# Kernel optimization log

Measured on AMD Instinct MI355X. Metric: run time of the kernel, lower is better.

Reference implementation:

```python
import jax, jax.numpy as jnp
import numpy as np

H = 1024      # hidden_size
I = 512       # moe_intermediate_size
E = 8         # n_routed_experts
K = 2         # num_experts_per_tok
SI = I * 2    # shared expert intermediate (n_shared_experts=2)
B, S = 2, 1024


def setup_inputs() -> dict:
    key = jax.random.key(0)
    ks = jax.random.split(key, 9)
    s = 0.02
    return {
        "x": jax.random.normal(ks[0], (B, S, H), jnp.float32),
        "gate_w": jax.random.normal(ks[1], (E, H), jnp.float32) * s,
        "lb_bias": jnp.zeros((E,), jnp.float32),
        "expert_gate_w": jax.random.normal(ks[2], (E, I, H), jnp.float32) * s,
        "expert_up_w": jax.random.normal(ks[3], (E, I, H), jnp.float32) * s,
        "expert_down_w": jax.random.normal(ks[4], (E, H, I), jnp.float32) * s,
        "shared_gate_w": jax.random.normal(ks[5], (SI, H), jnp.float32) * s,
        "shared_up_w": jax.random.normal(ks[6], (SI, H), jnp.float32) * s,
        "shared_down_w": jax.random.normal(ks[7], (H, SI), jnp.float32) * s,
    }


def _mlp(x, gw, uw, dw):
    # SwiGLU: down( silu(gate(x)) * up(x) )
    return (jax.nn.silu(x @ gw.T) * (x @ uw.T)) @ dw.T


def reference(x, gate_w, lb_bias, expert_gate_w, expert_up_w, expert_down_w,
              shared_gate_w, shared_up_w, shared_down_w):
    b, s, h = x.shape
    xf = x.reshape(-1, h)                                   # [T, H]
    # --- SimpleRouter (sigmoid scoring) ---
    logits = xf @ gate_w.T + lb_bias                        # [T, E]
    scores = jax.nn.sigmoid(logits.astype(jnp.float32))
    topw, topi = jax.lax.top_k(scores, K)                   # [T, K]
    topw = (topw / (topw.sum(-1, keepdims=True) + 1e-8)).astype(x.dtype)
    # --- _process_local: per-expert dispatch/compute/combine ---
    # Faithful to torch source: expert_weights[mask].mean(dim=-1) collapses to a
    # SCALAR per expert (mean routing weight over all tokens sent to that expert).
    out = jnp.zeros_like(xf)
    for e in range(E):
        m = (topi == e)                                     # [T, K]
        sel = m.any(axis=-1)                                # [T]
        cnt = m.sum()
        wmean = (topw * m).sum() / jnp.maximum(cnt, 1).astype(topw.dtype)
        y = _mlp(xf, expert_gate_w[e], expert_up_w[e], expert_down_w[e])  # [T, H]
        out = out + jnp.where(sel[:, None], y * wmean, jnp.zeros((), x.dtype))
    out = out.reshape(b, s, h)
    # --- shared experts ---
    out = out + _mlp(x, shared_gate_w, shared_up_w, shared_down_w)
    return out
```

## Files before the change

kernel.cpp:

```cpp
#include <hip/hip_runtime.h>

#define H_DIM 1024
#define I_DIM 512
#define NE 8
#define SI_DIM 1024
#define NT 2048
#define NS 4096

typedef __bf16 bf16;
typedef __bf16 bf16x4 __attribute__((ext_vector_type(4)));
typedef __bf16 bf16x8 __attribute__((ext_vector_type(8)));
typedef float f32x4 __attribute__((ext_vector_type(4)));

#define W_GU 0
#define W_DN 8388608ull
#define W_SGU 12582912ull
#define W_SDN 14680064ull
#define W_TOT 15728640ull

#define NWB 15360
#define NXB 2048
#define NRB 512

#define OFF_CNT 0
#define OFF_WM 64
#define OFF_BASE 128
#define OFF_TOPI 1024
#define OFF_TOPW (OFF_TOPI + NT * 8)
#define OFF_GSLOT (OFF_TOPW + NT * 8)
#define OFF_LISTS (OFF_GSLOT + NT * 8)
#define OFF_WB (OFF_LISTS + NS * 4)
#define OFF_XB (OFF_WB + W_TOT * 2)
#define OFF_ACTE (OFF_XB + (size_t)NT * H_DIM * 2)
#define OFF_ACTS (OFF_ACTE + (size_t)(NS + 128) * I_DIM * 2)
#define OFF_YDE (OFF_ACTS + (size_t)NT * SI_DIM * 2)
#define OFF_YDS (OFF_YDE + (size_t)NS * H_DIM * 2)

__device__ __forceinline__ bf16x4 cvt4(f32x4 v) {
  bf16x4 r;
  r.x = (bf16)v.x; r.y = (bf16)v.y; r.z = (bf16)v.z; r.w = (bf16)v.w;
  return r;
}

__device__ __forceinline__ void glds16(const bf16* g, bf16* l) {
  __builtin_amdgcn_global_load_lds(
      (const __attribute__((address_space(1))) unsigned int*)g,
      (__attribute__((address_space(3))) unsigned int*)l, 16, 0, 0);
}

__global__ __launch_bounds__(256) void prep_kernel(
    const float* __restrict__ x, const float* __restrict__ gw,
    const float* __restrict__ lb, const float* __restrict__ eg,
    const float* __restrict__ eu, const float* __restrict__ ed,
    const float* __restrict__ sg, const float* __restrict__ su,
    const float* __restrict__ sd, bf16* __restrict__ wb,
    bf16* __restrict__ xb, int2* __restrict__ topi,
    float2* __restrict__ topw) {
  const int bx = blockIdx.x;
  const int tid = threadIdx.x;
  if (bx < NWB) {
    size_t i = ((size_t)bx * 256 + tid) * 4;
    const float* src;
    if (i < W_DN) {
      size_t z = i >> 20;
      int rem = (int)(i & ((1u << 20) - 1));
      int rp = rem >> 10, k = rem & 1023;
      int b = rp >> 4;
      int sr = ((b >> 1) << 4) | (rp & 15);
      src = ((b & 1) ? eu : eg) + (z << 19) + ((size_t)sr << 10) + k;
    } else if (i < W_SGU) {
      src = ed + (i - W_DN);
    } else if (i < W_SDN) {
      int rem = (int)(i - W_SGU);
      int rp = rem >> 10, k = rem & 1023;
      int b = rp >> 4;
      int sr = ((b >> 1) << 4) | (rp & 15);
      src = ((b & 1) ? su : sg) + ((size_t)sr << 10) + k;
    } else {
      src = sd + (i - W_SDN);
    }
    *(bf16x4*)(wb + i) = cvt4(*(const f32x4*)src);
  } else if (bx < NWB + NXB) {
    size_t i = ((size_t)(bx - NWB) * 256 + tid) * 4;
    *(bf16x4*)(xb + i) = cvt4(*(const f32x4*)(x + i));
  } else {
    const int lane = tid & 63;
    const int t = (bx - NWB - NXB) * 4 + (tid >> 6);
    const float* xr = x + (size_t)t * H_DIM;
    float s[NE];
#pragma unroll
    for (int e = 0; e < NE; e++) s[e] = 0.f;
#pragma unroll
    for (int k0 = 0; k0 < H_DIM; k0 += 256) {
      f32x4 xv = *(const f32x4*)(xr + k0 + lane * 4);
#pragma unroll
      for (int e = 0; e < NE; e++) {
        f32x4 gv = *(const f32x4*)(gw + e * H_DIM + k0 + lane * 4);
        s[e] += xv.x * gv.x + xv.y * gv.y + xv.z * gv.z + xv.w * gv.w;
      }
    }
#pragma unroll
    for (int e = 0; e < NE; e++) {
      float v = s[e];
#pragma unroll
      for (int off = 32; off > 0; off >>= 1) v += __shfl_xor(v, off);
      s[e] = v;
    }
    if (lane == 0) {
      float sc[NE];
#pragma unroll
      for (int e = 0; e < NE; e++) sc[e] = 1.f / (1.f + expf(-(s[e] + lb[e])));
      int i1 = 0;
#pragma unroll
      for (int e = 1; e < NE; e++)
        if (sc[e] > sc[i1]) i1 = e;
      int i2 = -1;
#pragma unroll
      for (int e = 0; e < NE; e++) {
        if (e == i1) continue;
        if (i2 < 0 || sc[e] > sc[i2]) i2 = e;
      }
      float w1 = sc[i1], w2 = sc[i2];
      float inv = 1.f / (w1 + w2 + 1e-8f);
      topi[t] = make_int2(i1, i2);
      topw[t] = make_float2(w1 * inv, w2 * inv);
    }
  }
}

__global__ __launch_bounds__(512) void build_kernel(
    const int2* __restrict__ topi, const float2* __restrict__ topw,
    int* __restrict__ cnt, float* __restrict__ wm, int* __restrict__ base,
    int* __restrict__ lists, int2* __restrict__ gslot) {
  __shared__ int cnt_l[NE];
  __shared__ int base_l[NE + 1];
  const int e = threadIdx.x >> 6;
  const int lane = threadIdx.x & 63;

  int c = 0;
  float wacc = 0.f;
  for (int t0 = 0; t0 < NT; t0 += 64) {
    int2 ti = topi[t0 + lane];
    float2 tw = topw[t0 + lane];
    bool hit = (ti.x == e) || (ti.y == e);
    float w = (ti.x == e) ? tw.x : ((ti.y == e) ? tw.y : 0.f);
    c += __popcll(__ballot(hit));
#pragma unroll
    for (int off = 32; off > 0; off >>= 1) w += __shfl_xor(w, off);
    wacc += w;
  }
  if (lane == 0) {
    cnt_l[e] = c;
    cnt[e] = c;
    wm[e] = wacc / (float)(c > 0 ? c : 1);
  }
  __syncthreads();
  if (threadIdx.x == 0) {
    int b = 0;
    for (int i = 0; i < NE; i++) {
      base_l[i] = b;
      base[i] = b;
      b += cnt_l[i];
    }
    base[NE] = b;
  }
  __syncthreads();

  int pos = base_l[e];
  for (int t0 = 0; t0 < NT; t0 += 64) {
    int t = t0 + lane;
    int2 ti = topi[t];
    bool hit = (ti.x == e) || (ti.y == e);
    unsigned long long m = __ballot(hit);
    int pre = __popcll(m & ((1ull << lane) - 1ull));
    if (hit) {
      int g = pos + pre;
      lists[g] = t;
      if (ti.x == e) gslot[t].x = g;
      else gslot[t].y = g;
    }
    pos += __popcll(m);
  }
}

__global__ __launch_bounds__(256, 2) void gemm_gu(
    const bf16* __restrict__ wb, const bf16* __restrict__ xb,
    const int* __restrict__ cnt, const int* __restrict__ base,
    const int* __restrict__ lists, bf16* __restrict__ act_e,
    bf16* __restrict__ act_s) {
  const int z = blockIdx.z, ct = blockIdx.x, rt = blockIdx.y;
  const bf16* Bb;
  bf16* Cb;
  int mrem, ldc;
  __shared__ int rows_s[128];
  __shared__ __align__(16) bf16 As[128 * 64];
  __shared__ __align__(16) bf16 Bs[128 * 64];
  const int tid = threadIdx.x;
  if (z < NE) {
    if (ct >= 8) return;
    int c = cnt[z];
    if (rt * 128 >= c) return;
    int rb = base[z] + rt * 128;
    mrem = c - rt * 128;
    if (tid < 128) rows_s[tid] = lists[rb + (tid < mrem ? tid : mrem - 1)];
    Bb = wb + W_GU + ((size_t)z << 20) + (size_t)ct * 128 * H_DIM;
    Cb = act_e + (size_t)rb * I_DIM;
    ldc = I_DIM;
  } else {
    mrem = 128;
    if (tid < 128) rows_s[tid] = rt * 128 + tid;
    Bb = wb + W_SGU + (size_t)ct * 128 * H_DIM;
    Cb = act_s + (size_t)rt * 128 * SI_DIM;
    ldc = SI_DIM;
  }
  __syncthreads();

  const int lane = tid & 63, wave = tid >> 6;
  const int mw = (wave >> 1) * 64, nw = (wave & 1) * 64;
  const int l15 = lane & 15, quad = lane >> 4;
  const int srow = tid >> 3, scol = (tid & 7) * 8;

  const bf16* ap[4];
  const bf16* bp[4];
#pragma unroll
  for (int r = 0; r < 4; r++) {
    ap[r] = xb + (size_t)rows_s[srow + r * 32] * H_DIM + scol;
    bp[r] = Bb + (size_t)(srow + r * 32) * H_DIM + scol;
  }

  f32x4 acc[4][4] = {};
  for (int k0 = 0; k0 < H_DIM; k0 += 64) {
#pragma unroll
    for (int r = 0; r < 4; r++)
      glds16(ap[r] + k0, &As[(srow + r * 32) * 64 + scol]);
#pragma unroll
    for (int r = 0; r < 4; r++)
      glds16(bp[r] + k0, &Bs[(srow + r * 32) * 64 + scol]);
    __syncthreads();
#pragma unroll
    for (int kk = 0; kk < 2; kk++) {
      const int kof = kk * 32 + quad * 8;
      bf16x8 av[4], bv[4];
#pragma unroll
      for (int i = 0; i < 4; i++) {
        av[i] = *(const bf16x8*)&As[(mw + i * 16 + l15) * 64 + kof];
        bv[i] = *(const bf16x8*)&Bs[(nw + i * 16 + l15) * 64 + kof];
      }
#pragma unroll
      for (int i = 0; i < 4; i++)
#pragma unroll
        for (int j = 0; j < 4; j++)
          acc[i][j] = __builtin_amdgcn_mfma_f32_16x16x32_bf16(av[i], bv[j], acc[i][j], 0, 0, 0);
    }
    __syncthreads();
  }

#pragma unroll
  for (int i = 0; i < 4; i++) {
#pragma unroll
    for (int rg = 0; rg < 4; rg++) {
      int rl = mw + i * 16 + quad * 4 + rg;
      if (rl < mrem) {
#pragma unroll
        for (int jp = 0; jp < 2; jp++) {
          float g = acc[i][jp * 2][rg];
          float u = acc[i][jp * 2 + 1][rg];
          int c = ct * 64 + (nw >> 1) + jp * 16 + l15;
          Cb[(size_t)rl * ldc + c] = (bf16)((g / (1.f + __expf(-g))) * u);
        }
      }
    }
  }
}

__global__ __launch_bounds__(256, 2) void gemm_down(
    const bf16* __restrict__ wb, const bf16* __restrict__ act_e,
    const bf16* __restrict__ act_s, const int* __restrict__ cnt,
    const int* __restrict__ base, bf16* __restrict__ yd_e,
    bf16* __restrict__ yd_s) {
  const int z = blockIdx.z, ct = blockIdx.x, rt = blockIdx.y;
  const bf16 *Ab, *Bb;
  bf16* Cb;
  int K, mrem;
  if (z < NE) {
    int c = cnt[z];
    if (rt * 128 >= c) return;
    int rb = base[z] + rt * 128;
    mrem = c - rt * 128;
    Ab = act_e + (size_t)rb * I_DIM;
    K = I_DIM;
    Bb = wb + W_DN + ((size_t)z << 19) + (size_t)ct * 128 * I_DIM;
    Cb = yd_e + (size_t)rb * H_DIM + ct * 128;
  } else {
    mrem = 128;
    Ab = act_s + (size_t)rt * 128 * SI_DIM;
    K = SI_DIM;
    Bb = wb + W_SDN + (size_t)ct * 128 * SI_DIM;
    Cb = yd_s + (size_t)rt * 128 * H_DIM + ct * 128;
  }

  __shared__ __align__(16) bf16 As[128 * 64];
  __shared__ __align__(16) bf16 Bs[128 * 64];

  const int tid = threadIdx.x;
  const int lane = tid & 63, wave = tid >> 6;
  const int mw = (wave >> 1) * 64, nw = (wave & 1) * 64;
  const int l15 = lane & 15, quad = lane >> 4;
  const int srow = tid >> 3, scol = (tid & 7) * 8;

  f32x4 acc[4][4] = {};
  for (int k0 = 0; k0 < K; k0 += 64) {
#pragma unroll
    for (int r = 0; r < 4; r++)
      glds16(Ab + (size_t)(srow + r * 32) * K + k0 + scol,
             &As[(srow + r * 32) * 64 + scol]);
#pragma unroll
    for (int r = 0; r < 4; r++)
      glds16(Bb + (size_t)(srow + r * 32) * K + k0 + scol,
             &Bs[(srow + r * 32) * 64 + scol]);
    __syncthreads();
#pragma unroll
    for (int kk = 0; kk < 2; kk++) {
      const int kof = kk * 32 + quad * 8;
      bf16x8 av[4], bv[4];
#pragma unroll
      for (int i = 0; i < 4; i++) {
        av[i] = *(const bf16x8*)&As[(mw + i * 16 + l15) * 64 + kof];
        bv[i] = *(const bf16x8*)&Bs[(nw + i * 16 + l15) * 64 + kof];
      }
#pragma unroll
      for (int i = 0; i < 4; i++)
#pragma unroll
        for (int j = 0; j < 4; j++)
          acc[i][j] = __builtin_amdgcn_mfma_f32_16x16x32_bf16(av[i], bv[j], acc[i][j], 0, 0, 0);
    }
    __syncthreads();
  }

#pragma unroll
  for (int i = 0; i < 4; i++) {
#pragma unroll
    for (int rg = 0; rg < 4; rg++) {
      int rl = mw + i * 16 + quad * 4 + rg;
      if (rl < mrem) {
#pragma unroll
        for (int j = 0; j < 4; j++)
          Cb[(size_t)rl * H_DIM + nw + j * 16 + l15] = (bf16)acc[i][j][rg];
      }
    }
  }
}

__global__ __launch_bounds__(256) void combine_kernel(
    const bf16* __restrict__ yd_e, const bf16* __restrict__ yd_s,
    const int2* __restrict__ topi, const int2* __restrict__ gslot,
    const float* __restrict__ wm, float* __restrict__ out) {
  int t = blockIdx.x;
  int2 ei = topi[t];
  int2 gi = gslot[t];
  float w1 = wm[ei.x], w2 = wm[ei.y];
  int c = threadIdx.x * 4;
  bf16x4 y1 = *(const bf16x4*)(yd_e + (size_t)gi.x * H_DIM + c);
  bf16x4 y2 = *(const bf16x4*)(yd_e + (size_t)gi.y * H_DIM + c);
  bf16x4 ys = *(const bf16x4*)(yd_s + (size_t)t * H_DIM + c);
  f32x4 o;
  o.x = w1 * (float)y1.x + w2 * (float)y2.x + (float)ys.x;
  o.y = w1 * (float)y1.y + w2 * (float)y2.y + (float)ys.y;
  o.z = w1 * (float)y1.z + w2 * (float)y2.z + (float)ys.z;
  o.w = w1 * (float)y1.w + w2 * (float)y2.w + (float)ys.w;
  *(f32x4*)(out + (size_t)t * H_DIM + c) = o;
}

extern "C" void kernel_launch(void* const* d_in, const int* in_sizes, int n_in,
                              void* d_out, int out_size, void* d_ws,
                              size_t ws_size, hipStream_t stream) {
  (void)in_sizes; (void)n_in; (void)out_size; (void)ws_size;
  const float* x  = (const float*)d_in[0];
  const float* gw = (const float*)d_in[1];
  const float* lb = (const float*)d_in[2];
  const float* eg = (const float*)d_in[3];
  const float* eu = (const float*)d_in[4];
  const float* ed = (const float*)d_in[5];
  const float* sg = (const float*)d_in[6];
  const float* su = (const float*)d_in[7];
  const float* sd = (const float*)d_in[8];
  float* out = (float*)d_out;
  char* ws = (char*)d_ws;

  int* cnt     = (int*)(ws + OFF_CNT);
  float* wm    = (float*)(ws + OFF_WM);
  int* base    = (int*)(ws + OFF_BASE);
  int2* topi   = (int2*)(ws + OFF_TOPI);
  float2* topw = (float2*)(ws + OFF_TOPW);
  int2* gslot  = (int2*)(ws + OFF_GSLOT);
  int* lists   = (int*)(ws + OFF_LISTS);
  bf16* wb     = (bf16*)(ws + OFF_WB);
  bf16* xb     = (bf16*)(ws + OFF_XB);
  bf16* act_e  = (bf16*)(ws + OFF_ACTE);
  bf16* act_s  = (bf16*)(ws + OFF_ACTS);
  bf16* yd_e   = (bf16*)(ws + OFF_YDE);
  bf16* yd_s   = (bf16*)(ws + OFF_YDS);

  prep_kernel<<<NWB + NXB + NRB, 256, 0, stream>>>(x, gw, lb, eg, eu, ed, sg,
                                                   su, sd, wb, xb, topi, topw);
  build_kernel<<<1, 512, 0, stream>>>(topi, topw, cnt, wm, base, lists, gslot);
  gemm_gu<<<dim3(16, 16, 9), 256, 0, stream>>>(wb, xb, cnt, base, lists, act_e,
                                               act_s);
  gemm_down<<<dim3(8, 16, 9), 256, 0, stream>>>(wb, act_e, act_s, cnt, base,
                                                yd_e, yd_s);
  combine_kernel<<<NT, 256, 0, stream>>>(yd_e, yd_s, topi, gslot, wm, out);
}
```

Baseline: 224.9 us.

## Fuse weight conversion into GEMMs, scatter-add down outputs, drop combine kernel

The separate pass that converted all weights to bf16 is removed. The GEMMs now read fp32 weights directly, convert them in registers and write them to LDS, and the x conversion is folded into the router kernel. The build kernel is parallelised across experts using fixed per-expert list slots, and LDS tiles get an XOR swizzle to avoid bank conflicts. The down GEMM applies the expert mean weight and atomically adds into a zeroed fp32 output, which removes the bf16 intermediate buffers and the combine kernel. The trade-off is twice the global bytes on the weight loads, register-path loads in place of direct global-to-LDS copies for B, and atomic contention on the output.

```diff
diff --git a/kernel.cpp b/kernel.cpp
--- a/kernel.cpp
+++ b/kernel.cpp
@@ -12,29 +12,14 @@
 typedef __bf16 bf16x8 __attribute__((ext_vector_type(8)));
 typedef float f32x4 __attribute__((ext_vector_type(4)));
 
-#define W_GU 0
-#define W_DN 8388608ull
-#define W_SGU 12582912ull
-#define W_SDN 14680064ull
-#define W_TOT 15728640ull
-
-#define NWB 15360
-#define NXB 2048
-#define NRB 512
-
 #define OFF_CNT 0
 #define OFF_WM 64
-#define OFF_BASE 128
 #define OFF_TOPI 1024
 #define OFF_TOPW (OFF_TOPI + NT * 8)
-#define OFF_GSLOT (OFF_TOPW + NT * 8)
-#define OFF_LISTS (OFF_GSLOT + NT * 8)
-#define OFF_WB (OFF_LISTS + NS * 4)
-#define OFF_XB (OFF_WB + W_TOT * 2)
+#define OFF_LISTS (OFF_TOPW + NT * 8)
+#define OFF_XB (OFF_LISTS + NE * NT * 4)
 #define OFF_ACTE (OFF_XB + (size_t)NT * H_DIM * 2)
-#define OFF_ACTS (OFF_ACTE + (size_t)(NS + 128) * I_DIM * 2)
-#define OFF_YDE (OFF_ACTS + (size_t)NT * SI_DIM * 2)
-#define OFF_YDS (OFF_YDE + (size_t)NS * H_DIM * 2)
+#define OFF_ACTS (OFF_ACTE + (size_t)NE * NT * I_DIM * 2)
 
 __device__ __forceinline__ bf16x4 cvt4(f32x4 v) {
   bf16x4 r;
@@ -42,104 +27,81 @@
   return r;
 }
 
+__device__ __forceinline__ bf16x8 cvt8(f32x4 a, f32x4 b) {
+  bf16x8 r;
+  r[0] = (bf16)a.x; r[1] = (bf16)a.y; r[2] = (bf16)a.z; r[3] = (bf16)a.w;
+  r[4] = (bf16)b.x; r[5] = (bf16)b.y; r[6] = (bf16)b.z; r[7] = (bf16)b.w;
+  return r;
+}
+
 __device__ __forceinline__ void glds16(const bf16* g, bf16* l) {
   __builtin_amdgcn_global_load_lds(
       (const __attribute__((address_space(1))) unsigned int*)g,
       (__attribute__((address_space(3))) unsigned int*)l, 16, 0, 0);
 }
 
-__global__ __launch_bounds__(256) void prep_kernel(
+__global__ __launch_bounds__(256) void router_kernel(
     const float* __restrict__ x, const float* __restrict__ gw,
-    const float* __restrict__ lb, const float* __restrict__ eg,
-    const float* __restrict__ eu, const float* __restrict__ ed,
-    const float* __restrict__ sg, const float* __restrict__ su,
-    const float* __restrict__ sd, bf16* __restrict__ wb,
-    bf16* __restrict__ xb, int2* __restrict__ topi,
-    float2* __restrict__ topw) {
-  const int bx = blockIdx.x;
-  const int tid = threadIdx.x;
-  if (bx < NWB) {
-    size_t i = ((size_t)bx * 256 + tid) * 4;
-    const float* src;
-    if (i < W_DN) {
-      size_t z = i >> 20;
-      int rem = (int)(i & ((1u << 20) - 1));
-      int rp = rem >> 10, k = rem & 1023;
-      int b = rp >> 4;
-      int sr = ((b >> 1) << 4) | (rp & 15);
-      src = ((b & 1) ? eu : eg) + (z << 19) + ((size_t)sr << 10) + k;
-    } else if (i < W_SGU) {
-      src = ed + (i - W_DN);
-    } else if (i < W_SDN) {
-      int rem = (int)(i - W_SGU);
-      int rp = rem >> 10, k = rem & 1023;
-      int b = rp >> 4;
-      int sr = ((b >> 1) << 4) | (rp & 15);
-      src = ((b & 1) ? su : sg) + ((size_t)sr << 10) + k;
-    } else {
-      src = sd + (i - W_SDN);
-    }
-    *(bf16x4*)(wb + i) = cvt4(*(const f32x4*)src);
-  } else if (bx < NWB + NXB) {
-    size_t i = ((size_t)(bx - NWB) * 256 + tid) * 4;
-    *(bf16x4*)(xb + i) = cvt4(*(const f32x4*)(x + i));
-  } else {
-    const int lane = tid & 63;
-    const int t = (bx - NWB - NXB) * 4 + (tid >> 6);
-    const float* xr = x + (size_t)t * H_DIM;
-    float s[NE];
-#pragma unroll
-    for (int e = 0; e < NE; e++) s[e] = 0.f;
-#pragma unroll
-    for (int k0 = 0; k0 < H_DIM; k0 += 256) {
-      f32x4 xv = *(const f32x4*)(xr + k0 + lane * 4);
-#pragma unroll
-      for (int e = 0; e < NE; e++) {
-        f32x4 gv = *(const f32x4*)(gw + e * H_DIM + k0 + lane * 4);
-        s[e] += xv.x * gv.x + xv.y * gv.y + xv.z * gv.z + xv.w * gv.w;
-      }
-    }
+    const float* __restrict__ lb, bf16* __restrict__ xb,
+    int2* __restrict__ topi, float2* __restrict__ topw) {
+  const int lane = threadIdx.x & 63;
+  const int t = blockIdx.x * 4 + (threadIdx.x >> 6);
+  const float* xr = x + (size_t)t * H_DIM;
+  bf16* xw = xb + (size_t)t * H_DIM;
+
+  float s[NE];
+#pragma unroll
+  for (int e = 0; e < NE; e++) s[e] = 0.f;
+#pragma unroll
+  for (int k0 = 0; k0 < H_DIM; k0 += 256) {
+    f32x4 xv = *(const f32x4*)(xr + k0 + lane * 4);
+    *(bf16x4*)(xw + k0 + lane * 4) = cvt4(xv);
 #pragma unroll
     for (int e = 0; e < NE; e++) {
-      float v = s[e];
-#pragma unroll
-      for (int off = 32; off > 0; off >>= 1) v += __shfl_xor(v, off);
-      s[e] = v;
-    }
-    if (lane == 0) {
-      float sc[NE];
-#pragma unroll
-      for (int e = 0; e < NE; e++) sc[e] = 1.f / (1.f + expf(-(s[e] + lb[e])));
-      int i1 = 0;
-#pragma unroll
-      for (int e = 1; e < NE; e++)
-        if (sc[e] > sc[i1]) i1 = e;
-      int i2 = -1;
-#pragma unroll
-      for (int e = 0; e < NE; e++) {
-        if (e == i1) continue;
-        if (i2 < 0 || sc[e] > sc[i2]) i2 = e;
-      }
-      float w1 = sc[i1], w2 = sc[i2];
-      float inv = 1.f / (w1 + w2 + 1e-8f);
-      topi[t] = make_int2(i1, i2);
-      topw[t] = make_float2(w1 * inv, w2 * inv);
-    }
-  }
-}
-
-__global__ __launch_bounds__(512) void build_kernel(
+      f32x4 gv = *(const f32x4*)(gw + e * H_DIM + k0 + lane * 4);
+      s[e] += xv.x * gv.x + xv.y * gv.y + xv.z * gv.z + xv.w * gv.w;
+    }
+  }
+#pragma unroll
+  for (int e = 0; e < NE; e++) {
+    float v = s[e];
+#pragma unroll
+    for (int off = 32; off > 0; off >>= 1) v += __shfl_xor(v, off);
+    s[e] = v;
+  }
+  if (lane == 0) {
+    float sc[NE];
+#pragma unroll
+    for (int e = 0; e < NE; e++) sc[e] = 1.f / (1.f + expf(-(s[e] + lb[e])));
+    int i1 = 0;
+#pragma unroll
+    for (int e = 1; e < NE; e++)
+      if (sc[e] > sc[i1]) i1 = e;
+    int i2 = -1;
+#pragma unroll
+    for (int e = 0; e < NE; e++) {
+      if (e == i1) continue;
+      if (i2 < 0 || sc[e] > sc[i2]) i2 = e;
+    }
+    float w1 = sc[i1], w2 = sc[i2];
+    float inv = 1.f / (w1 + w2 + 1e-8f);
+    topi[t] = make_int2(i1, i2);
+    topw[t] = make_float2(w1 * inv, w2 * inv);
+  }
+}
+
+__global__ __launch_bounds__(256) void build_kernel(
     const int2* __restrict__ topi, const float2* __restrict__ topw,
-    int* __restrict__ cnt, float* __restrict__ wm, int* __restrict__ base,
-    int* __restrict__ lists, int2* __restrict__ gslot) {
-  __shared__ int cnt_l[NE];
-  __shared__ int base_l[NE + 1];
-  const int e = threadIdx.x >> 6;
-  const int lane = threadIdx.x & 63;
+    int* __restrict__ cnt, float* __restrict__ wm, int* __restrict__ lists) {
+  const int e = blockIdx.x;
+  const int wave = threadIdx.x >> 6, lane = threadIdx.x & 63;
+  __shared__ int wc[4];
+  __shared__ float wf[4];
+  const int tbeg = wave * (NT / 4), tend = tbeg + NT / 4;
 
   int c = 0;
-  float wacc = 0.f;
-  for (int t0 = 0; t0 < NT; t0 += 64) {
+  float wa = 0.f;
+  for (int t0 = tbeg; t0 < tend; t0 += 64) {
     int2 ti = topi[t0 + lane];
     float2 tw = topw[t0 + lane];
     bool hit = (ti.x == e) || (ti.y == e);
@@ -147,69 +109,58 @@
     c += __popcll(__ballot(hit));
 #pragma unroll
     for (int off = 32; off > 0; off >>= 1) w += __shfl_xor(w, off);
-    wacc += w;
-  }
-  if (lane == 0) {
-    cnt_l[e] = c;
-    cnt[e] = c;
-    wm[e] = wacc / (float)(c > 0 ? c : 1);
-  }
+    wa += w;
+  }
+  if (lane == 0) { wc[wave] = c; wf[wave] = wa; }
   __syncthreads();
-  if (threadIdx.x == 0) {
-    int b = 0;
-    for (int i = 0; i < NE; i++) {
-      base_l[i] = b;
-      base[i] = b;
-      b += cnt_l[i];
-    }
-    base[NE] = b;
-  }
-  __syncthreads();
-
-  int pos = base_l[e];
-  for (int t0 = 0; t0 < NT; t0 += 64) {
+  int pos = 0;
+  for (int w = 0; w < wave; w++) pos += wc[w];
+  for (int t0 = tbeg; t0 < tend; t0 += 64) {
     int t = t0 + lane;
     int2 ti = topi[t];
     bool hit = (ti.x == e) || (ti.y == e);
     unsigned long long m = __ballot(hit);
     int pre = __popcll(m & ((1ull << lane) - 1ull));
-    if (hit) {
-      int g = pos + pre;
-      lists[g] = t;
-      if (ti.x == e) gslot[t].x = g;
-      else gslot[t].y = g;
-    }
+    if (hit) lists[e * NT + pos + pre] = t;
     pos += __popcll(m);
   }
+  if (threadIdx.x == 0) {
+    int ctot = wc[0] + wc[1] + wc[2] + wc[3];
+    cnt[e] = ctot;
+    wm[e] = (wf[0] + wf[1] + wf[2] + wf[3]) / (float)(ctot > 0 ? ctot : 1);
+  }
 }
 
 __global__ __launch_bounds__(256, 2) void gemm_gu(
-    const bf16* __restrict__ wb, const bf16* __restrict__ xb,
-    const int* __restrict__ cnt, const int* __restrict__ base,
+    const float* __restrict__ eg, const float* __restrict__ eu,
+    const float* __restrict__ sg, const float* __restrict__ su,
+    const bf16* __restrict__ xb, const int* __restrict__ cnt,
     const int* __restrict__ lists, bf16* __restrict__ act_e,
     bf16* __restrict__ act_s) {
   const int z = blockIdx.z, ct = blockIdx.x, rt = blockIdx.y;
-  const bf16* Bb;
-  bf16* Cb;
-  int mrem, ldc;
+  const int tid = threadIdx.x;
   __shared__ int rows_s[128];
   __shared__ __align__(16) bf16 As[128 * 64];
   __shared__ __align__(16) bf16 Bs[128 * 64];
-  const int tid = threadIdx.x;
+  int mrem, ldc;
+  bf16* Cb;
+  const float *Pg, *Pu;
   if (z < NE) {
     if (ct >= 8) return;
     int c = cnt[z];
     if (rt * 128 >= c) return;
-    int rb = base[z] + rt * 128;
     mrem = c - rt * 128;
-    if (tid < 128) rows_s[tid] = lists[rb + (tid < mrem ? tid : mrem - 1)];
-    Bb = wb + W_GU + ((size_t)z << 20) + (size_t)ct * 128 * H_DIM;
-    Cb = act_e + (size_t)rb * I_DIM;
+    if (tid < 128)
+      rows_s[tid] = lists[z * NT + rt * 128 + (tid < mrem ? tid : mrem - 1)];
+    Pg = eg + ((size_t)z << 19);
+    Pu = eu + ((size_t)z << 19);
+    Cb = act_e + ((size_t)z * NT + rt * 128) * I_DIM;
     ldc = I_DIM;
   } else {
     mrem = 128;
     if (tid < 128) rows_s[tid] = rt * 128 + tid;
-    Bb = wb + W_SGU + (size_t)ct * 128 * H_DIM;
+    Pg = sg;
+    Pu = su;
     Cb = act_s + (size_t)rt * 128 * SI_DIM;
     ldc = SI_DIM;
   }
@@ -218,33 +169,46 @@
   const int lane = tid & 63, wave = tid >> 6;
   const int mw = (wave >> 1) * 64, nw = (wave & 1) * 64;
   const int l15 = lane & 15, quad = lane >> 4;
-  const int srow = tid >> 3, scol = (tid & 7) * 8;
+  const int srow = tid >> 3;
+  const int cch = tid & 7;
+  const int p8 = cch * 8;
+  const int sx = (l15 & 7) * 8;
+  const int ctb = ct * 128;
 
   const bf16* ap[4];
-  const bf16* bp[4];
+  const float* bp[4];
+  int alo[4], blo[4];
 #pragma unroll
   for (int r = 0; r < 4; r++) {
-    ap[r] = xb + (size_t)rows_s[srow + r * 32] * H_DIM + scol;
-    bp[r] = Bb + (size_t)(srow + r * 32) * H_DIM + scol;
+    int R = srow + r * 32;
+    ap[r] = xb + (size_t)rows_s[R] * H_DIM + ((cch ^ (R & 7)) * 8);
+    alo[r] = R * 64 + p8;
+    int idx = ctb + R;
+    int b = idx >> 4;
+    int sr = ((b >> 1) << 4) | (idx & 15);
+    bp[r] = ((b & 1) ? Pu : Pg) + (size_t)sr * H_DIM + p8;
+    blo[r] = R * 64 + ((cch ^ (R & 7)) * 8);
   }
 
   f32x4 acc[4][4] = {};
   for (int k0 = 0; k0 < H_DIM; k0 += 64) {
 #pragma unroll
-    for (int r = 0; r < 4; r++)
-      glds16(ap[r] + k0, &As[(srow + r * 32) * 64 + scol]);
-#pragma unroll
-    for (int r = 0; r < 4; r++)
-      glds16(bp[r] + k0, &Bs[(srow + r * 32) * 64 + scol]);
+    for (int r = 0; r < 4; r++) glds16(ap[r] + k0, &As[alo[r]]);
+#pragma unroll
+    for (int r = 0; r < 4; r++) {
+      f32x4 v0 = *(const f32x4*)(bp[r] + k0);
+      f32x4 v1 = *(const f32x4*)(bp[r] + k0 + 4);
+      *(bf16x8*)&Bs[blo[r]] = cvt8(v0, v1);
+    }
     __syncthreads();
 #pragma unroll
     for (int kk = 0; kk < 2; kk++) {
-      const int kof = kk * 32 + quad * 8;
+      const int ko = (kk * 4 + quad) * 8;
       bf16x8 av[4], bv[4];
 #pragma unroll
       for (int i = 0; i < 4; i++) {
-        av[i] = *(const bf16x8*)&As[(mw + i * 16 + l15) * 64 + kof];
-        bv[i] = *(const bf16x8*)&Bs[(nw + i * 16 + l15) * 64 + kof];
+        av[i] = *(const bf16x8*)&As[(mw + i * 16 + l15) * 64 + (ko ^ sx)];
+        bv[i] = *(const bf16x8*)&Bs[(nw + i * 16 + l15) * 64 + (ko ^ sx)];
       }
 #pragma unroll
       for (int i = 0; i < 4; i++)
@@ -274,59 +238,75 @@
 }
 
 __global__ __launch_bounds__(256, 2) void gemm_down(
-    const bf16* __restrict__ wb, const bf16* __restrict__ act_e,
-    const bf16* __restrict__ act_s, const int* __restrict__ cnt,
-    const int* __restrict__ base, bf16* __restrict__ yd_e,
-    bf16* __restrict__ yd_s) {
+    const float* __restrict__ ed, const float* __restrict__ sd,
+    const bf16* __restrict__ act_e, const bf16* __restrict__ act_s,
+    const int* __restrict__ cnt, const float* __restrict__ wm,
+    const int* __restrict__ lists, float* __restrict__ out) {
   const int z = blockIdx.z, ct = blockIdx.x, rt = blockIdx.y;
-  const bf16 *Ab, *Bb;
-  bf16* Cb;
+  const int tid = threadIdx.x;
+  __shared__ int rows_s[128];
+  __shared__ __align__(16) bf16 As[128 * 64];
+  __shared__ __align__(16) bf16 Bs[128 * 64];
   int K, mrem;
+  const bf16* Ab;
+  const float* Bbase;
   if (z < NE) {
     int c = cnt[z];
     if (rt * 128 >= c) return;
-    int rb = base[z] + rt * 128;
     mrem = c - rt * 128;
-    Ab = act_e + (size_t)rb * I_DIM;
+    if (tid < 128)
+      rows_s[tid] = lists[z * NT + rt * 128 + (tid < mrem ? tid : mrem - 1)];
+    Ab = act_e + ((size_t)z * NT + rt * 128) * I_DIM;
     K = I_DIM;
-    Bb = wb + W_DN + ((size_t)z << 19) + (size_t)ct * 128 * I_DIM;
-    Cb = yd_e + (size_t)rb * H_DIM + ct * 128;
+    Bbase = ed + (size_t)z * H_DIM * I_DIM;
   } else {
     mrem = 128;
+    if (tid < 128) rows_s[tid] = rt * 128 + tid;
     Ab = act_s + (size_t)rt * 128 * SI_DIM;
     K = SI_DIM;
-    Bb = wb + W_SDN + (size_t)ct * 128 * SI_DIM;
-    Cb = yd_s + (size_t)rt * 128 * H_DIM + ct * 128;
-  }
-
-  __shared__ __align__(16) bf16 As[128 * 64];
-  __shared__ __align__(16) bf16 Bs[128 * 64];
-
-  const int tid = threadIdx.x;
+    Bbase = sd;
+  }
+  __syncthreads();
+
   const int lane = tid & 63, wave = tid >> 6;
   const int mw = (wave >> 1) * 64, nw = (wave & 1) * 64;
   const int l15 = lane & 15, quad = lane >> 4;
-  const int srow = tid >> 3, scol = (tid & 7) * 8;
+  const int srow = tid >> 3;
+  const int cch = tid & 7;
+  const int p8 = cch * 8;
+  const int sx = (l15 & 7) * 8;
+
+  const bf16* ap[4];
+  const float* bp[4];
+  int alo[4], blo[4];
+#pragma unroll
+  for (int r = 0; r < 4; r++) {
+    int R = srow + r * 32;
+    ap[r] = Ab + (size_t)R * K + ((cch ^ (R & 7)) * 8);
+    alo[r] = R * 64 + p8;
+    bp[r] = Bbase + (size_t)(ct * 128 + R) * K + p8;
+    blo[r] = R * 64 + ((cch ^ (R & 7)) * 8);
+  }
 
   f32x4 acc[4][4] = {};
   for (int k0 = 0; k0 < K; k0 += 64) {
 #pragma unroll
-    for (int r = 0; r < 4; r++)
-      glds16(Ab + (size_t)(srow + r * 32) * K + k0 + scol,
-             &As[(srow + r * 32) * 64 + scol]);
-#pragma unroll
-    for (int r = 0; r < 4; r++)
-      glds16(Bb + (size_t)(srow + r * 32) * K + k0 + scol,
-             &Bs[(srow + r * 32) * 64 + scol]);
+    for (int r = 0; r < 4; r++) glds16(ap[r] + k0, &As[alo[r]]);
+#pragma unroll
+    for (int r = 0; r < 4; r++) {
+      f32x4 v0 = *(const f32x4*)(bp[r] + k0);
+      f32x4 v1 = *(const f32x4*)(bp[r] + k0 + 4);
+      *(bf16x8*)&Bs[blo[r]] = cvt8(v0, v1);
+    }
     __syncthreads();
 #pragma unroll
     for (int kk = 0; kk < 2; kk++) {
-      const int kof = kk * 32 + quad * 8;
+      const int ko = (kk * 4 + quad) * 8;
       bf16x8 av[4], bv[4];
 #pragma unroll
       for (int i = 0; i < 4; i++) {
-        av[i] = *(const bf16x8*)&As[(mw + i * 16 + l15) * 64 + kof];
-        bv[i] = *(const bf16x8*)&Bs[(nw + i * 16 + l15) * 64 + kof];
+        av[i] = *(const bf16x8*)&As[(mw + i * 16 + l15) * 64 + (ko ^ sx)];
+        bv[i] = *(const bf16x8*)&Bs[(nw + i * 16 + l15) * 64 + (ko ^ sx)];
       }
 #pragma unroll
       for (int i = 0; i < 4; i++)
@@ -337,38 +317,21 @@
     __syncthreads();
   }
 
+  const float wsc = (z < NE) ? wm[z] : 1.f;
 #pragma unroll
   for (int i = 0; i < 4; i++) {
 #pragma unroll
     for (int rg = 0; rg < 4; rg++) {
       int rl = mw + i * 16 + quad * 4 + rg;
       if (rl < mrem) {
+        int t = rows_s[rl];
+        float* orow = out + (size_t)t * H_DIM + ct * 128 + nw;
 #pragma unroll
         for (int j = 0; j < 4; j++)
-          Cb[(size_t)rl * H_DIM + nw + j * 16 + l15] = (bf16)acc[i][j][rg];
+          atomicAdd(&orow[j * 16 + l15], wsc * acc[i][j][rg]);
       }
     }
   }
-}
-
-__global__ __launch_bounds__(256) void combine_kernel(
-    const bf16* __restrict__ yd_e, const bf16* __restrict__ yd_s,
-    const int2* __restrict__ topi, const int2* __restrict__ gslot,
-    const float* __restrict__ wm, float* __restrict__ out) {
-  int t = blockIdx.x;
-  int2 ei = topi[t];
-  int2 gi = gslot[t];
-  float w1 = wm[ei.x], w2 = wm[ei.y];
-  int c = threadIdx.x * 4;
-  bf16x4 y1 = *(const bf16x4*)(yd_e + (size_t)gi.x * H_DIM + c);
-  bf16x4 y2 = *(const bf16x4*)(yd_e + (size_t)gi.y * H_DIM + c);
-  bf16x4 ys = *(const bf16x4*)(yd_s + (size_t)t * H_DIM + c);
-  f32x4 o;
-  o.x = w1 * (float)y1.x + w2 * (float)y2.x + (float)ys.x;
-  o.y = w1 * (float)y1.y + w2 * (float)y2.y + (float)ys.y;
-  o.z = w1 * (float)y1.z + w2 * (float)y2.z + (float)ys.z;
-  o.w = w1 * (float)y1.w + w2 * (float)y2.w + (float)ys.w;
-  *(f32x4*)(out + (size_t)t * H_DIM + c) = o;
 }
 
 extern "C" void kernel_launch(void* const* d_in, const int* in_sizes, int n_in,
@@ -389,24 +352,18 @@
 
   int* cnt     = (int*)(ws + OFF_CNT);
   float* wm    = (float*)(ws + OFF_WM);
-  int* base    = (int*)(ws + OFF_BASE);
   int2* topi   = (int2*)(ws + OFF_TOPI);
   float2* topw = (float2*)(ws + OFF_TOPW);
-  int2* gslot  = (int2*)(ws + OFF_GSLOT);
   int* lists   = (int*)(ws + OFF_LISTS);
-  bf16* wb     = (bf16*)(ws + OFF_WB);
   bf16* xb     = (bf16*)(ws + OFF_XB);
   bf16* act_e  = (bf16*)(ws + OFF_ACTE);
   bf16* act_s  = (bf16*)(ws + OFF_ACTS);
-  bf16* yd_e   = (bf16*)(ws + OFF_YDE);
-  bf16* yd_s   = (bf16*)(ws + OFF_YDS);
-
-  prep_kernel<<<NWB + NXB + NRB, 256, 0, stream>>>(x, gw, lb, eg, eu, ed, sg,
-                                                   su, sd, wb, xb, topi, topw);
-  build_kernel<<<1, 512, 0, stream>>>(topi, topw, cnt, wm, base, lists, gslot);
-  gemm_gu<<<dim3(16, 16, 9), 256, 0, stream>>>(wb, xb, cnt, base, lists, act_e,
-                                               act_s);
-  gemm_down<<<dim3(8, 16, 9), 256, 0, stream>>>(wb, act_e, act_s, cnt, base,
-                                                yd_e, yd_s);
-  combine_kernel<<<NT, 256, 0, stream>>>(yd_e, yd_s, topi, gslot, wm, out);
-}
+
+  hipMemsetAsync(d_out, 0, (size_t)NT * H_DIM * sizeof(float), stream);
+  router_kernel<<<NT / 4, 256, 0, stream>>>(x, gw, lb, xb, topi, topw);
+  build_kernel<<<NE, 256, 0, stream>>>(topi, topw, cnt, wm, lists);
+  gemm_gu<<<dim3(16, 16, 9), 256, 0, stream>>>(eg, eu, sg, su, xb, cnt, lists,
+                                               act_e, act_s);
+  gemm_down<<<dim3(8, 16, 9), 256, 0, stream>>>(ed, sd, act_e, act_s, cnt, wm,
+                                                lists, out);
+}
```

After: 209.6 us. 1.07x faster.
